# Optimization experiments

Measured on AMD Instinct MI355X. Metric: run time of the kernel, lower is better.

Reference implementation:

```python
import jax, jax.numpy as jnp
import numpy as np

EMB = 64
NEG = 0.2  # DGL GATConv default negative_slope

def seg_sum(x, ids, n):
    return jax.ops.segment_sum(x, ids, num_segments=n)

def seg_max(x, ids, n):
    return jax.ops.segment_max(x, ids, num_segments=n)

def gat(x, src, dst, W, al, ar):
    # DGL GATConv: fc (no bias), per-head additive attention, edge softmax over in-edges of dst
    N = x.shape[0]
    H, D = al.shape
    h = (x @ W).reshape(N, H, D)                 # (N,H,D)
    el = jnp.sum(h * al, -1)                     # (N,H)
    er = jnp.sum(h * ar, -1)                     # (N,H)
    e = jax.nn.leaky_relu(el[src] + er[dst], negative_slope=NEG)  # (E,H)
    m = seg_max(e, dst, N)
    ex = jnp.exp(e - m[dst])
    den = seg_sum(ex, dst, N)
    alpha = ex / den[dst]                        # (E,H)
    return seg_sum(alpha[..., None] * h[src], dst, N)  # (N,H,D)

def conv1d(x, w, b):
    y = jax.lax.conv_general_dilated(x, w, (1,), 'VALID', dimension_numbers=('NCH', 'OIH', 'NCH'))
    return y + b[None, :, None]

def maxpool1d(x, k, s):
    return jax.lax.reduce_window(x, -jnp.inf, jax.lax.max, (1, 1, k), (1, 1, s), 'VALID')

def textcnn(pad_dmap, c1w, c1b, c2w, c2b, c3w, c3b):
    x = jnp.squeeze(pad_dmap, 1).transpose(0, 2, 1)   # (B, emb, L)
    x = maxpool1d(conv1d(x, c1w, c1b), 3, 3)
    x = maxpool1d(conv1d(x, c2w, c2b), 3, 3)
    x = maxpool1d(conv1d(x, c3w, c3b), 130, 1)        # (B,128,1)
    return jnp.squeeze(x, 2)

def branch(feat, src, dst, nid, pad_dmap, ng, p):
    g = jax.nn.relu(gat(feat, src, dst, p['Wg1'], p['al1'], p['ar1'])).reshape(-1, EMB * 3)
    g = jax.nn.relu(gat(g, src, dst, p['Wg2'], p['al2'], p['ar2'])).reshape(-1, EMB * 9)
    g = jax.nn.relu(gat(g, src, dst, p['Wg3'], p['al3'], p['ar3'])).reshape(-1, EMB * 9)
    gmax = seg_max(g, nid, ng)                        # graph-level MaxPooling readout
    g = jax.nn.relu(gmax @ p['fcg_w'] + p['fcg_b'])
    s = textcnn(pad_dmap, p['c1w'], p['c1b'], p['c2w'], p['c2b'], p['c3w'], p['c3b'])
    s = jax.nn.relu(s @ p['tf_w'] + p['tf_b'])
    w = jax.nn.sigmoid(p['w1'])
    return (1.0 - w) * g + w * s

PKEYS = ['Wg1', 'al1', 'ar1', 'Wg2', 'al2', 'ar2', 'Wg3', 'al3', 'ar3', 'fcg_w', 'fcg_b',
         'c1w', 'c1b', 'c2w', 'c2b', 'c3w', 'c3b', 'tf_w', 'tf_b', 'w1',
         'fc1_w', 'fc1_b', 'fc2_w', 'fc2_b', 'out_w', 'out_b']

def forward(feat1, feat2, pad_dmap1, pad_dmap2, params, src1, dst1, src2, dst2, nid1, nid2, num_graphs):
    p = dict(zip(PKEYS, params))
    gc1 = branch(feat1, src1, dst1, nid1, pad_dmap1, num_graphs, p)
    gc2 = branch(feat2, src2, dst2, nid2, pad_dmap2, num_graphs, p)
    gc = jnp.concatenate([gc1, gc2], axis=1)
    gc = jax.nn.relu(gc @ p['fc1_w'] + p['fc1_b'])   # dropout is identity at eval
    gc = jax.nn.relu(gc @ p['fc2_w'] + p['fc2_b'])
    return jax.nn.sigmoid(gc @ p['out_w'] + p['out_b'])

def setup_inputs() -> dict:
    key = jax.random.key(0)
    ks = jax.random.split(key, 40)
    N, E, B, L = 8000, 160000, 16, 1200
    d = {}
    d['feat1'] = jax.random.normal(ks[0], (N, EMB), jnp.float32)
    d['feat2'] = jax.random.normal(ks[1], (N, EMB), jnp.float32)
    d['pad_dmap1'] = jax.random.normal(ks[2], (B, 1, L, EMB), jnp.float32)
    d['pad_dmap2'] = jax.random.normal(ks[3], (B, 1, L, EMB), jnp.float32)
    d['src1'] = jax.random.randint(ks[4], (E,), 0, N, jnp.int32)
    d['dst1'] = jax.random.randint(ks[5], (E,), 0, N, jnp.int32)
    d['src2'] = jax.random.randint(ks[6], (E,), 0, N, jnp.int32)
    d['dst2'] = jax.random.randint(ks[7], (E,), 0, N, jnp.int32)
    nid = ((jnp.arange(N) * B) // N).astype(jnp.int32)  # sorted, all graphs non-empty
    d['nid1'] = nid
    d['nid2'] = nid
    d['num_graphs'] = B
    def lin(k, i, o):
        return jax.random.normal(k, (i, o), jnp.float32) * np.float32(1.0 / np.sqrt(i))
    d['Wg1'] = lin(ks[8], EMB, EMB * 3)
    d['al1'] = jax.random.normal(ks[9], (3, EMB), jnp.float32) * 0.1
    d['ar1'] = jax.random.normal(ks[10], (3, EMB), jnp.float32) * 0.1
    d['Wg2'] = lin(ks[11], EMB * 3, EMB * 9)
    d['al2'] = jax.random.normal(ks[12], (3, EMB * 3), jnp.float32) * 0.1
    d['ar2'] = jax.random.normal(ks[13], (3, EMB * 3), jnp.float32) * 0.1
    d['Wg3'] = lin(ks[14], EMB * 9, EMB * 9)
    d['al3'] = jax.random.normal(ks[15], (1, EMB * 9), jnp.float32) * 0.1
    d['ar3'] = jax.random.normal(ks[16], (1, EMB * 9), jnp.float32) * 0.1
    d['fcg_w'] = lin(ks[17], EMB * 9, 128)
    d['fcg_b'] = jnp.zeros((128,), jnp.float32)
    d['c1w'] = jax.random.normal(ks[18], (128, EMB, 3), jnp.float32) * np.float32(1.0 / np.sqrt(EMB * 3))
    d['c1b'] = jnp.zeros((128,), jnp.float32)
    d['c2w'] = jax.random.normal(ks[19], (128, 128, 3), jnp.float32) * np.float32(1.0 / np.sqrt(128 * 3))
    d['c2b'] = jnp.zeros((128,), jnp.float32)
    d['c3w'] = jax.random.normal(ks[20], (128, 128, 3), jnp.float32) * np.float32(1.0 / np.sqrt(128 * 3))
    d['c3b'] = jnp.zeros((128,), jnp.float32)
    d['tf_w'] = lin(ks[21], 128, 128)
    d['tf_b'] = jnp.zeros((128,), jnp.float32)
    d['w1'] = jnp.full((1,), 0.5, jnp.float32)
    d['fc1_w'] = lin(ks[22], 256, 512)
    d['fc1_b'] = jnp.zeros((512,), jnp.float32)
    d['fc2_w'] = lin(ks[23], 512, 256)
    d['fc2_b'] = jnp.zeros((256,), jnp.float32)
    d['out_w'] = lin(ks[24], 256, 1)
    d['out_b'] = jnp.zeros((1,), jnp.float32)
    return d

def reference(feat1, src1, dst1, nid1, pad_dmap1, feat2, src2, dst2, nid2, pad_dmap2, num_graphs,
              Wg1, al1, ar1, Wg2, al2, ar2, Wg3, al3, ar3, fcg_w, fcg_b,
              c1w, c1b, c2w, c2b, c3w, c3b, tf_w, tf_b, w1,
              fc1_w, fc1_b, fc2_w, fc2_b, out_w, out_b):
    params = (Wg1, al1, ar1, Wg2, al2, ar2, Wg3, al3, ar3, fcg_w, fcg_b,
              c1w, c1b, c2w, c2b, c3w, c3b, tf_w, tf_b, w1,
              fc1_w, fc1_b, fc2_w, fc2_b, out_w, out_b)
    return forward(feat1, feat2, pad_dmap1, pad_dmap2, params, src1, dst1, src2, dst2, nid1, nid2, num_graphs)
```

## Files before the change

### kernel.cpp

```cpp
#include <hip/hip_runtime.h>
#include <hip/hip_bf16.h>
#include <math.h>

#define NEG_SLOPE 0.2f

__global__ void zero_i32(int* __restrict__ p, int n) {
    int i = blockIdx.x * blockDim.x + threadIdx.x;
    if (i < n) p[i] = 0;
}

__global__ void count_edges2(const int* __restrict__ dst0, const int* __restrict__ dst1,
                             int* __restrict__ cnt, int N, int E) {
    int i = blockIdx.x * blockDim.x + threadIdx.x;
    if (i >= 2 * E) return;
    int br = i >= E;
    int j = i - br * E;
    const int* d = br ? dst1 : dst0;
    atomicAdd(&cnt[br * N + d[j]], 1);
}

__global__ void scan_block(const int* __restrict__ cnt_all, int* __restrict__ rs_all, int N) {
    __shared__ int s[1024];
    int br = blockIdx.x;
    const int* cnt = cnt_all + br * N;
    int* rs = rs_all + br * (N + 1);
    int tid = threadIdx.x;
    int running = 0;
    for (int base = 0; base < N; base += 1024) {
        int v = (base + tid < N) ? cnt[base + tid] : 0;
        __syncthreads();
        s[tid] = v;
        __syncthreads();
        for (int off = 1; off < 1024; off <<= 1) {
            int t = (tid >= off) ? s[tid - off] : 0;
            __syncthreads();
            if (tid >= off) s[tid] += t;
            __syncthreads();
        }
        if (base + tid < N) rs[base + tid] = running + s[tid] - v;
        running += s[1023];
    }
    if (tid == 0) rs[N] = running;
}

__global__ void scatter_edges2(const int* __restrict__ dst0, const int* __restrict__ dst1,
                               const int* __restrict__ rs_all, int* __restrict__ fill_all,
                               int* __restrict__ eidx_all, int N, int E) {
    int i = blockIdx.x * blockDim.x + threadIdx.x;
    if (i >= 2 * E) return;
    int br = i >= E;
    int j = i - br * E;
    const int* d = br ? dst1 : dst0;
    int dd = d[j];
    int pos = atomicAdd(&fill_all[br * N + dd], 1);
    eidx_all[br * E + rs_all[br * (N + 1) + dd] + pos] = j;
}

__device__ __forceinline__ short f2bf(float x) {
    __hip_bfloat16 h = __float2bfloat16(x);
    return *reinterpret_cast<short*>(&h);
}
__device__ __forceinline__ float bf2f(short s) {
    unsigned int u = ((unsigned int)(unsigned short)s) << 16;
    return __uint_as_float(u);
}
__device__ __forceinline__ float us2f(unsigned short s) {
    return __uint_as_float((unsigned int)s << 16);
}

__global__ void split_bf2_w(const float* __restrict__ W, short* __restrict__ W2t, int K, int N) {
    int idx = blockIdx.x * blockDim.x + threadIdx.x;
    if (idx >= K * N) return;
    int k = idx / N, n = idx - k * N;
    float x = W[idx];
    short hs = f2bf(x);
    short ls = f2bf(x - bf2f(hs));
    size_t base = (size_t)n * 2 * K;
    W2t[base + k] = hs;
    W2t[base + K + k] = ls;
}

__global__ void split_bf2_cw(const float* __restrict__ w, short* __restrict__ w2, int Kp) {
    int idx = blockIdx.x * blockDim.x + threadIdx.x;
    if (idx >= 128 * Kp) return;
    int o = idx / Kp, k = idx - o * Kp;
    float x = w[idx];
    short hs = f2bf(x);
    short ls = f2bf(x - bf2f(hs));
    size_t base = (size_t)o * 2 * Kp;
    w2[base + k] = hs;
    w2[base + Kp + k] = ls;
}

typedef __attribute__((ext_vector_type(8))) short short8;
typedef __attribute__((ext_vector_type(4))) short short4v;
typedef __attribute__((ext_vector_type(4))) float floatx4;

__global__ __launch_bounds__(256) void gemm_bf3_v4(const float* __restrict__ A0,
                                                   const float* __restrict__ A1,
                                                   const short* __restrict__ Bt,
                                                   unsigned short* __restrict__ Cbf,
                                                   int M, int K, int N, size_t cBrStride) {
    __shared__ __align__(16) short sA[64 * 72];
    __shared__ __align__(16) short sB[192 * 72];
    int tid = threadIdx.x;
    int wave = tid >> 6, lane = tid & 63;
    int m = lane & 15, q = lane >> 4;
    int row0 = blockIdx.y << 6;
    int col0 = blockIdx.x * 192;
    const float* A = blockIdx.z ? A1 : A0;
    unsigned short* Cbfb = Cbf + blockIdx.z * cBrStride;
    int K2 = K * 2;
    floatx4 acc[4][3];
#pragma unroll
    for (int rt = 0; rt < 4; ++rt)
#pragma unroll
        for (int ct = 0; ct < 3; ++ct) acc[rt][ct] = (floatx4){0.f, 0.f, 0.f, 0.f};

    for (int k0 = 0; k0 < K; k0 += 32) {
#pragma unroll
        for (int p = 0; p < 2; ++p) {
            int t = tid + (p << 8);
            int r = t >> 3, c = (t & 7) << 2;
            float4 av = *(const float4*)&A[(size_t)(row0 + r) * K + k0 + c];
            short4v hs, ls;
            hs[0] = f2bf(av.x); ls[0] = f2bf(av.x - bf2f(hs[0]));
            hs[1] = f2bf(av.y); ls[1] = f2bf(av.y - bf2f(hs[1]));
            hs[2] = f2bf(av.z); ls[2] = f2bf(av.z - bf2f(hs[2]));
            hs[3] = f2bf(av.w); ls[3] = f2bf(av.w - bf2f(hs[3]));
            *(short4v*)&sA[r * 72 + c] = hs;
            *(short4v*)&sA[r * 72 + 32 + c] = ls;
        }
#pragma unroll
        for (int p = 0; p < 6; ++p) {
            int t = tid + (p << 8);
            int n = t >> 3, sub = t & 7;
            int srcoff = k0 + (sub << 3) + ((sub >= 4) ? (K - 32) : 0);
            *(float4*)&sB[n * 72 + (sub << 3)] =
                *(const float4*)&Bt[(size_t)(col0 + n) * K2 + srcoff];
        }
        __syncthreads();
        short8 a_hi[4], a_lo[4];
#pragma unroll
        for (int rt = 0; rt < 4; ++rt) {
            a_hi[rt] = *(const short8*)&sA[(rt * 16 + m) * 72 + q * 8];
            a_lo[rt] = *(const short8*)&sA[(rt * 16 + m) * 72 + 32 + q * 8];
        }
#pragma unroll
        for (int ct = 0; ct < 3; ++ct) {
            short8 b_hi = *(const short8*)&sB[(wave * 48 + ct * 16 + m) * 72 + q * 8];
            short8 b_lo = *(const short8*)&sB[(wave * 48 + ct * 16 + m) * 72 + 32 + q * 8];
#pragma unroll
            for (int rt = 0; rt < 4; ++rt) {
                acc[rt][ct] = __builtin_amdgcn_mfma_f32_16x16x32_bf16(a_hi[rt], b_hi, acc[rt][ct], 0, 0, 0);
                acc[rt][ct] = __builtin_amdgcn_mfma_f32_16x16x32_bf16(a_lo[rt], b_hi, acc[rt][ct], 0, 0, 0);
                acc[rt][ct] = __builtin_amdgcn_mfma_f32_16x16x32_bf16(a_hi[rt], b_lo, acc[rt][ct], 0, 0, 0);
            }
        }
        __syncthreads();
    }
#pragma unroll
    for (int rt = 0; rt < 4; ++rt)
#pragma unroll
        for (int ct = 0; ct < 3; ++ct)
#pragma unroll
            for (int r = 0; r < 4; ++r) {
                size_t idx = (size_t)(row0 + rt * 16 + q * 4 + r) * N + col0 + wave * 48 + ct * 16 + m;
                Cbfb[idx] = (unsigned short)f2bf(acc[rt][ct][r]);
            }
}

__global__ void gat_elr(const unsigned short* __restrict__ h, const float* __restrict__ al,
                        const float* __restrict__ ar, float* __restrict__ el,
                        float* __restrict__ er, int N, int H, int D,
                        size_t hBr, size_t eBr) {
    int wid = (blockIdx.x * blockDim.x + threadIdx.x) >> 6;
    int lane = threadIdx.x & 63;
    if (wid >= 2 * N * H) return;
    int br = wid / (N * H);
    int loc = wid - br * N * H;
    int n = loc / H, hh = loc - n * H;
    const unsigned short* hp = h + br * hBr + ((size_t)n * H + hh) * D;
    const float* alp = al + (size_t)hh * D;
    const float* arp = ar + (size_t)hh * D;
    float sl = 0.f, sr = 0.f;
    for (int d = lane; d < D; d += 64) {
        float v = us2f(hp[d]);
        sl += v * alp[d];
        sr += v * arp[d];
    }
    for (int off = 32; off > 0; off >>= 1) {
        sl += __shfl_down(sl, off, 64);
        sr += __shfl_down(sr, off, 64);
    }
    if (lane == 0) { el[br * eBr + loc] = sl; er[br * eBr + loc] = sr; }
}

__device__ __forceinline__ float lrelu(float v) {
    return (v > 0.f) ? v : NEG_SLOPE * v;
}

__global__ void gat_softmax_wave(const float* __restrict__ el_all, const float* __restrict__ er_all,
                                 const int* __restrict__ src0, const int* __restrict__ src1,
                                 const int* __restrict__ rs_all, const int* __restrict__ eidx_all,
                                 float* __restrict__ alpha_all, int N, int H, int E,
                                 size_t eBr, size_t aBr) {
    int g = (blockIdx.x * blockDim.x + threadIdx.x) >> 6;
    int lane = threadIdx.x & 63;
    if (g >= 2 * N) return;
    int br = g / N;
    int n = g - br * N;
    const int* src = br ? src1 : src0;
    const int* rs = rs_all + br * (N + 1);
    const int* eidx = eidx_all + br * E;
    const float* el = el_all + br * eBr;
    const float* er = er_all + br * eBr;
    float* alpha = alpha_all + br * aBr;
    int s0 = rs[n], s1 = rs[n + 1];
    int deg = s1 - s0;
    if (deg == 0) return;
    float ern0 = er[n * H + 0];
    float ern1 = (H > 1) ? er[n * H + 1] : 0.f;
    float ern2 = (H > 2) ? er[n * H + 2] : 0.f;
    if (deg <= 64) {
        int e = 0, s = 0;
        float v0 = -INFINITY, v1 = -INFINITY, v2 = -INFINITY;
        if (lane < deg) {
            e = eidx[s0 + lane];
            s = src[e];
            v0 = lrelu(el[s * H + 0] + ern0);
            if (H > 1) {
                v1 = lrelu(el[s * H + 1] + ern1);
                v2 = lrelu(el[s * H + 2] + ern2);
            }
        }
        float m0 = v0, m1 = v1, m2 = v2;
#pragma unroll
        for (int off = 32; off > 0; off >>= 1) {
            m0 = fmaxf(m0, __shfl_xor(m0, off, 64));
            m1 = fmaxf(m1, __shfl_xor(m1, off, 64));
            m2 = fmaxf(m2, __shfl_xor(m2, off, 64));
        }
        float ex0 = (lane < deg) ? expf(v0 - m0) : 0.f;
        float ex1 = (lane < deg && H > 1) ? expf(v1 - m1) : 0.f;
        float ex2 = (lane < deg && H > 2) ? expf(v2 - m2) : 0.f;
        float d0 = ex0, d1 = ex1, d2 = ex2;
#pragma unroll
        for (int off = 32; off > 0; off >>= 1) {
            d0 += __shfl_xor(d0, off, 64);
            d1 += __shfl_xor(d1, off, 64);
            d2 += __shfl_xor(d2, off, 64);
        }
        if (lane < deg) {
            alpha[(size_t)e * H + 0] = ex0 / d0;
            if (H > 1) {
                alpha[(size_t)e * H + 1] = ex1 / d1;
                alpha[(size_t)e * H + 2] = ex2 / d2;
            }
        }
    } else {
        float m0 = -INFINITY, m1 = -INFINITY, m2 = -INFINITY;
        for (int j = s0 + lane; j < s1; j += 64) {
            int e = eidx[j], s = src[e];
            float v0 = lrelu(el[s * H + 0] + ern0);
            alpha[(size_t)e * H + 0] = v0; m0 = fmaxf(m0, v0);
            if (H > 1) {
                float v1 = lrelu(el[s * H + 1] + ern1);
                float v2 = lrelu(el[s * H + 2] + ern2);
                alpha[(size_t)e * H + 1] = v1; m1 = fmaxf(m1, v1);
                alpha[(size_t)e * H + 2] = v2; m2 = fmaxf(m2, v2);
            }
        }
#pragma unroll
        for (int off = 32; off > 0; off >>= 1) {
            m0 = fmaxf(m0, __shfl_xor(m0, off, 64));
            m1 = fmaxf(m1, __shfl_xor(m1, off, 64));
            m2 = fmaxf(m2, __shfl_xor(m2, off, 64));
        }
        float d0 = 0.f, d1 = 0.f, d2 = 0.f;
        for (int j = s0 + lane; j < s1; j += 64) {
            int e = eidx[j];
            float ex0 = expf(alpha[(size_t)e * H + 0] - m0);
            alpha[(size_t)e * H + 0] = ex0; d0 += ex0;
            if (H > 1) {
                float ex1 = expf(alpha[(size_t)e * H + 1] - m1);
                float ex2 = expf(alpha[(size_t)e * H + 2] - m2);
                alpha[(size_t)e * H + 1] = ex1; d1 += ex1;
                alpha[(size_t)e * H + 2] = ex2; d2 += ex2;
            }
        }
#pragma unroll
        for (int off = 32; off > 0; off >>= 1) {
            d0 += __shfl_xor(d0, off, 64);
            d1 += __shfl_xor(d1, off, 64);
            d2 += __shfl_xor(d2, off, 64);
        }
        float i0 = 1.f / d0;
        float i1 = (H > 1) ? 1.f / d1 : 0.f;
        float i2 = (H > 2) ? 1.f / d2 : 0.f;
        for (int j = s0 + lane; j < s1; j += 64) {
            int e = eidx[j];
            alpha[(size_t)e * H + 0] *= i0;
            if (H > 1) {
                alpha[(size_t)e * H + 1] *= i1;
                alpha[(size_t)e * H + 2] *= i2;
            }
        }
    }
}

#define TILE_E 64
__global__ void gat_aggregate(const unsigned short* __restrict__ hb_all,
                              const float* __restrict__ alpha_all,
                              const int* __restrict__ src0, const int* __restrict__ src1,
                              const int* __restrict__ rs_all, const int* __restrict__ eidx_all,
                              float4* __restrict__ out4_all, int N, int H, int D, int E,
                              size_t hBr, size_t aBr, size_t o4Br) {
    __shared__ int s_src[TILE_E];
    __shared__ float s_alpha[TILE_E * 3];
    int n = blockIdx.x;
    int br = blockIdx.y;
    const int* src = br ? src1 : src0;
    const int* rs = rs_all + br * (N + 1);
    const int* eidx = eidx_all + br * E;
    const unsigned short* hb = hb_all + br * hBr;
    const float* alpha = alpha_all + br * aBr;
    float4* out4 = out4_all + br * o4Br;
    int HD = H * D;
    int HD4 = HD >> 2;
    int tid = threadIdx.x;
    int s0 = rs[n], s1 = rs[n + 1];
    bool active = tid < HD4;
    int hh = active ? (tid << 2) / D : 0;
    float4 acc = {0.f, 0.f, 0.f, 0.f};
    for (int base = s0; base < s1; base += TILE_E) {
        int cntE = s1 - base; if (cntE > TILE_E) cntE = TILE_E;
        if (tid < cntE) {
            int e = eidx[base + tid];
            s_src[tid] = src[e];
#pragma unroll
            for (int h = 0; h < 3; ++h)
                if (h < H) s_alpha[tid * 3 + h] = alpha[(size_t)e * H + h];
        }
        __syncthreads();
        if (active) {
#pragma unroll 4
            for (int i = 0; i < cntE; ++i) {
                float a = s_alpha[i * 3 + hh];
                ushort4 hv = *(const ushort4*)&hb[(size_t)s_src[i] * HD + (tid << 2)];
                acc.x += a * us2f(hv.x);
                acc.y += a * us2f(hv.y);
                acc.z += a * us2f(hv.z);
                acc.w += a * us2f(hv.w);
            }
        }
        __syncthreads();
    }
    if (active) {
        acc.x = fmaxf(acc.x, 0.f); acc.y = fmaxf(acc.y, 0.f);
        acc.z = fmaxf(acc.z, 0.f); acc.w = fmaxf(acc.w, 0.f);
        out4[(size_t)n * HD4 + tid] = acc;
    }
}

__global__ void seg_max_atomic(const float* __restrict__ g_all, const int* __restrict__ nid,
                               int* __restrict__ out_all, int N, int C,
                               size_t gBr, size_t oBr) {
    int br = blockIdx.y;
    const float* g = g_all + br * gBr;
    int* out = out_all + br * oBr;
    int n0 = blockIdx.x << 5;
    int n1 = n0 + 32; if (n1 > N) n1 = N;
    if (n0 >= N) return;
    for (int c = threadIdx.x; c < C; c += blockDim.x) {
        int cur = nid[n0];
        float m = 0.f;
        for (int n = n0; n < n1; ++n) {
            int gid = nid[n];
            if (gid != cur) {
                atomicMax(&out[cur * C + c], __float_as_int(m));
                cur = gid; m = 0.f;
            }
            m = fmaxf(m, g[(size_t)n * C + c]);
        }
        atomicMax(&out[cur * C + c], __float_as_int(m));
    }
}

__global__ void linear_wave(const float* __restrict__ in, const float* __restrict__ W,
                            const float* __restrict__ bias, float* __restrict__ out,
                            int K, int O, int act, size_t inBr, size_t outBr) {
    int o = blockIdx.x * 4 + (threadIdx.x >> 6);
    int b = blockIdx.y;
    int lane = threadIdx.x & 63;
    if (o >= O) return;
    const float* ip = in + blockIdx.z * inBr + (size_t)b * K;
    float acc = 0.f;
    for (int k = lane; k < K; k += 64)
        acc += ip[k] * W[(size_t)k * O + o];
    for (int off = 32; off > 0; off >>= 1)
        acc += __shfl_down(acc, off, 64);
    if (lane == 0) {
        acc += bias[o];
        if (act == 1) acc = fmaxf(acc, 0.f);
        else if (act == 2) acc = 1.f / (1.f + expf(-acc));
        out[blockIdx.z * outBr + (size_t)b * O + o] = acc;
    }
}

__global__ void transpose_pad2(const float* __restrict__ pad0, const float* __restrict__ pad1,
                               float* __restrict__ xT, int B, int L, int C) {
    int idx = blockIdx.x * blockDim.x + threadIdx.x;
    int per = B * L * C;
    if (idx >= 2 * per) return;
    int br = idx >= per;
    int loc = idx - br * per;
    const float* pad = br ? pad1 : pad0;
    int l = loc % L;
    int c = (loc / L) % C;
    int b = loc / (L * C);
    xT[idx] = pad[((size_t)b * L + l) * C + c];
}

__global__ __launch_bounds__(256) void conv_mfma(const float* __restrict__ x,
                                                 const short* __restrict__ w2,
                                                 const float* __restrict__ bias,
                                                 float* __restrict__ y,
                                                 int Cin, int Lin, int Lout,
                                                 size_t xBr, size_t yBr) {
    extern __shared__ __align__(16) char smem[];
    float* sx = (float*)smem;
    short* sB = (short*)(smem + (size_t)Cin * 68 * 4);
    int Kp = Cin * 3;
    int K2 = Kp * 2;
    int b = blockIdx.y;
    const float* xb = x + blockIdx.z * xBr + (size_t)b * Cin * Lin;
    float* yb = y + blockIdx.z * yBr + (size_t)b * 128 * Lout;
    int l0 = blockIdx.x << 6;
    int tid = threadIdx.x;
    int wave = tid >> 6, lane = tid & 63;
    int m = lane & 15, q = lane >> 4;
    int wrow = (wave & 1) << 5;
    int wcol = (wave >> 1) << 6;
    int loadL = Lin - l0; if (loadL > 66) loadL = 66;
    for (int idx = tid; idx < Cin * loadL; idx += 256) {
        int c = idx / loadL, i = idx - c * loadL;
        sx[c * 68 + i] = xb[(size_t)c * Lin + l0 + i];
    }
    floatx4 acc[2][4];
#pragma unroll
    for (int rt = 0; rt < 2; ++rt)
#pragma unroll
        for (int ct = 0; ct < 4; ++ct) acc[rt][ct] = (floatx4){0.f, 0.f, 0.f, 0.f};

    for (int k0 = 0; k0 < Kp; k0 += 32) {
#pragma unroll
        for (int p = 0; p < 4; ++p) {
            int t = tid + (p << 8);
            int o = t >> 3, slot = t & 7;
            int srcoff = k0 + ((slot & 3) << 3) + ((slot >= 4) ? Kp : 0);
            *(float4*)&sB[o * 72 + (slot << 3)] = *(const float4*)&w2[(size_t)o * K2 + srcoff];
        }
        __syncthreads();
        short8 a_hi[2], a_lo[2];
#pragma unroll
        for (int rt = 0; rt < 2; ++rt) {
            int pos = wrow + rt * 16 + m;
#pragma unroll
            for (int kk = 0; kk < 8; ++kk) {
                int k = k0 + q * 8 + kk;
                int c = k / 3, j = k - c * 3;
                float v = sx[c * 68 + pos + j];
                short hv = f2bf(v);
                a_hi[rt][kk] = hv;
                a_lo[rt][kk] = f2bf(v - bf2f(hv));
            }
        }
#pragma unroll
        for (int ct = 0; ct < 4; ++ct) {
            short8 b_hi = *(const short8*)&sB[(wcol + ct * 16 + m) * 72 + q * 8];
            short8 b_lo = *(const short8*)&sB[(wcol + ct * 16 + m) * 72 + 32 + q * 8];
#pragma unroll
            for (int rt = 0; rt < 2; ++rt) {
                acc[rt][ct] = __builtin_amdgcn_mfma_f32_16x16x32_bf16(a_hi[rt], b_hi, acc[rt][ct], 0, 0, 0);
                acc[rt][ct] = __builtin_amdgcn_mfma_f32_16x16x32_bf16(a_lo[rt], b_hi, acc[rt][ct], 0, 0, 0);
                acc[rt][ct] = __builtin_amdgcn_mfma_f32_16x16x32_bf16(a_hi[rt], b_lo, acc[rt][ct], 0, 0, 0);
            }
        }
        __syncthreads();
    }
#pragma unroll
    for (int ct = 0; ct < 4; ++ct) {
        int o = wcol + ct * 16 + m;
        float bv = bias[o];
#pragma unroll
        for (int rt = 0; rt < 2; ++rt)
#pragma unroll
            for (int r = 0; r < 4; ++r) {
                int pos = wrow + rt * 16 + q * 4 + r;
                if (l0 + pos < Lout)
                    yb[(size_t)o * Lout + l0 + pos] = acc[rt][ct][r] + bv;
            }
    }
}

__global__ void maxpool(const float* __restrict__ y, float* __restrict__ p,
                        int BC, int Lin, int k, int s, int Lout) {
    int idx = blockIdx.x * blockDim.x + threadIdx.x;
    if (idx >= BC * Lout) return;
    int lo = idx % Lout, bc = idx / Lout;
    const float* yp = y + (size_t)bc * Lin + lo * s;
    float m = -INFINITY;
    for (int i = 0; i < k; ++i) m = fmaxf(m, yp[i]);
    p[idx] = m;
}

__global__ void combine_branch2(const float* __restrict__ g, const float* __restrict__ s,
                                const float* __restrict__ w1, float* __restrict__ cat, int B) {
    int idx = blockIdx.x * blockDim.x + threadIdx.x;
    int per = B * 128;
    if (idx >= 2 * per) return;
    int br = idx >= per;
    int loc = idx - br * per;
    int b = loc >> 7, c = loc & 127;
    float w = 1.f / (1.f + expf(-w1[0]));
    cat[b * 256 + br * 128 + c] = (1.f - w) * g[idx] + w * s[idx];
}

extern "C" void kernel_launch(void* const* d_in, const int* in_sizes, int n_in,
                              void* d_out, int out_size, void* d_ws, size_t ws_size,
                              hipStream_t stream) {
    const float* feat[2] = {(const float*)d_in[0], (const float*)d_in[1]};
    const float* pad[2]  = {(const float*)d_in[2], (const float*)d_in[3]};
    const int* src[2]    = {(const int*)d_in[4], (const int*)d_in[6]};
    const int* dst[2]    = {(const int*)d_in[5], (const int*)d_in[7]};
    const int* nid[2]    = {(const int*)d_in[8], (const int*)d_in[9]};
    const float* Wg[3]   = {(const float*)d_in[11], (const float*)d_in[14], (const float*)d_in[17]};
    const float* al[3]   = {(const float*)d_in[12], (const float*)d_in[15], (const float*)d_in[18]};
    const float* ar[3]   = {(const float*)d_in[13], (const float*)d_in[16], (const float*)d_in[19]};
    const float* fcg_w = (const float*)d_in[20]; const float* fcg_b = (const float*)d_in[21];
    const float* c1w = (const float*)d_in[22];   const float* c1b = (const float*)d_in[23];
    const float* c2w = (const float*)d_in[24];   const float* c2b = (const float*)d_in[25];
    const float* c3w = (const float*)d_in[26];   const float* c3b = (const float*)d_in[27];
    const float* tf_w = (const float*)d_in[28];  const float* tf_b = (const float*)d_in[29];
    const float* w1 = (const float*)d_in[30];
    const float* fc1_w = (const float*)d_in[31]; const float* fc1_b = (const float*)d_in[32];
    const float* fc2_w = (const float*)d_in[33]; const float* fc2_b = (const float*)d_in[34];
    const float* outw = (const float*)d_in[35];  const float* outb = (const float*)d_in[36];
    float* out = (float*)d_out;

    const int N = in_sizes[0] / 64;
    const int E = in_sizes[4];
    const int B = 16, L = 1200;
    const size_t NS = (size_t)N * 576;

    char* wsb = (char*)d_ws;
    size_t off = 0;
    auto allocB = [&](size_t bytes) -> void* {
        void* p = wsb + off;
        off += (bytes + 255) & ~(size_t)255;
        return p;
    };
    auto alloc = [&](size_t elems) -> void* { return allocB(elems * 4); };

    unsigned short* h_bf = (unsigned short*)allocB(2 * NS * 2);
    float* gA    = (float*)alloc(2 * NS);
    float* el    = (float*)alloc(2 * (size_t)N * 3);
    float* er    = (float*)alloc(2 * (size_t)N * 3);
    float* alpha = (float*)alloc(2 * (size_t)E * 3);
    int* rs      = (int*)alloc(2 * (N + 1));
    int* cnt     = (int*)alloc(2 * N);
    int* eidx    = (int*)alloc(2 * E);
    int* gmax    = (int*)alloc(2 * (size_t)B * 576);
    float* gvec  = (float*)alloc(2 * (size_t)B * 128);
    float* sp    = (float*)alloc(2 * (size_t)B * 128);
    float* sf    = (float*)alloc(2 * (size_t)B * 128);
    float* cat   = (float*)alloc((size_t)B * 256);
    float* f1    = (float*)alloc((size_t)B * 512);
    float* f2    = (float*)alloc((size_t)B * 256);
    short* w2t1  = (short*)allocB((size_t)192 * 2 * 64 * 2);
    short* w2t2  = (short*)allocB((size_t)576 * 2 * 192 * 2);
    short* w2t3  = (short*)allocB((size_t)576 * 2 * 576 * 2);
    short* cw1   = (short*)allocB((size_t)128 * 2 * 192 * 2);
    short* cw2   = (short*)allocB((size_t)128 * 2 * 384 * 2);
    short* cw3   = (short*)allocB((size_t)128 * 2 * 384 * 2);
    size_t tcnn_elems = 2 * ((size_t)B * 64 * L + (size_t)B * 128 * (1198 + 399 + 397 + 132 + 130));
    size_t uni_elems = 2 * NS > tcnn_elems ? 2 * NS : tcnn_elems;
    float* uni = (float*)alloc(uni_elems);
    float* gB = uni;
    float* xT = uni;
    float* y1 = xT + 2 * (size_t)B * 64 * L;
    float* p1 = y1 + 2 * (size_t)B * 128 * 1198;
    float* y2 = p1 + 2 * (size_t)B * 128 * 399;
    float* p2 = y2 + 2 * (size_t)B * 128 * 397;
    float* y3 = p2 + 2 * (size_t)B * 128 * 132;
    (void)ws_size; (void)n_in; (void)out_size;

    split_bf2_w<<<(64 * 192 + 255) / 256, 256, 0, stream>>>(Wg[0], w2t1, 64, 192);
    split_bf2_w<<<(192 * 576 + 255) / 256, 256, 0, stream>>>(Wg[1], w2t2, 192, 576);
    split_bf2_w<<<(576 * 576 + 255) / 256, 256, 0, stream>>>(Wg[2], w2t3, 576, 576);
    split_bf2_cw<<<(128 * 192 + 255) / 256, 256, 0, stream>>>(c1w, cw1, 192);
    split_bf2_cw<<<(128 * 384 + 255) / 256, 256, 0, stream>>>(c2w, cw2, 384);
    split_bf2_cw<<<(128 * 384 + 255) / 256, 256, 0, stream>>>(c3w, cw3, 384);
    short* w2t[3] = {w2t1, w2t2, w2t3};

    zero_i32<<<(2 * N + 255) / 256, 256, 0, stream>>>(cnt, 2 * N);
    count_edges2<<<(2 * E + 255) / 256, 256, 0, stream>>>(dst[0], dst[1], cnt, N, E);
    scan_block<<<2, 1024, 0, stream>>>(cnt, rs, N);
    zero_i32<<<(2 * N + 255) / 256, 256, 0, stream>>>(cnt, 2 * N);
    scatter_edges2<<<(2 * E + 255) / 256, 256, 0, stream>>>(dst[0], dst[1], rs, cnt, eidx, N, E);

    const int dims[3][3] = {{64, 3, 64}, {192, 3, 192}, {576, 1, 576}};
    float* outs[3] = {gA, gB, gA};
    const float* inp0 = feat[0];
    const float* inp1 = feat[1];
    for (int ly = 0; ly < 3; ++ly) {
        int K = dims[ly][0], H = dims[ly][1], D = dims[ly][2];
        int HD = H * D;
        gemm_bf3_v4<<<dim3(HD / 192, N / 64, 2), 256, 0, stream>>>(inp0, inp1, w2t[ly], h_bf,
                                                                   N, K, HD, NS);
        int waves2 = 2 * N * H;
        gat_elr<<<((size_t)waves2 * 64 + 255) / 256, 256, 0, stream>>>(h_bf, al[ly], ar[ly], el, er,
                                                                       N, H, D, NS, (size_t)N * 3);
        gat_softmax_wave<<<((size_t)2 * N * 64 + 255) / 256, 256, 0, stream>>>(
            el, er, src[0], src[1], rs, eidx, alpha, N, H, E, (size_t)N * 3, (size_t)E * 3);
        int aggThreads = (((HD >> 2) + 63) / 64) * 64;
        gat_aggregate<<<dim3(N, 2), aggThreads, 0, stream>>>(
            h_bf, alpha, src[0], src[1], rs, eidx, (float4*)outs[ly],
            N, H, D, E, NS, (size_t)E * 3, NS / 4);
        inp0 = outs[ly];
        inp1 = outs[ly] + NS;
    }
    zero_i32<<<(2 * B * 576 + 255) / 256, 256, 0, stream>>>(gmax, 2 * B * 576);
    seg_max_atomic<<<dim3((N + 31) / 32, 2), 256, 0, stream>>>(gA, nid[0], gmax, N, 576,
                                                               NS, (size_t)B * 576);
    linear_wave<<<dim3(32, B, 2), 256, 0, stream>>>((const float*)gmax, fcg_w, fcg_b, gvec,
                                                    576, 128, 1, (size_t)B * 576, (size_t)B * 128);

    transpose_pad2<<<((2 * B * 64 * L) + 255) / 256, 256, 0, stream>>>(pad[0], pad[1], xT, B, L, 64);
    conv_mfma<<<dim3(19, B, 2), 256, 64 * 68 * 4 + 128 * 72 * 2, stream>>>(
        xT, cw1, c1b, y1, 64, 1200, 1198, (size_t)B * 64 * L, (size_t)B * 128 * 1198);
    maxpool<<<(2 * B * 128 * 399 + 255) / 256, 256, 0, stream>>>(y1, p1, 2 * B * 128, 1198, 3, 3, 399);
    conv_mfma<<<dim3(7, B, 2), 256, 128 * 68 * 4 + 128 * 72 * 2, stream>>>(
        p1, cw2, c2b, y2, 128, 399, 397, (size_t)B * 128 * 399, (size_t)B * 128 * 397);
    maxpool<<<(2 * B * 128 * 132 + 255) / 256, 256, 0, stream>>>(y2, p2, 2 * B * 128, 397, 3, 3, 132);
    conv_mfma<<<dim3(3, B, 2), 256, 128 * 68 * 4 + 128 * 72 * 2, stream>>>(
        p2, cw3, c3b, y3, 128, 132, 130, (size_t)B * 128 * 132, (size_t)B * 128 * 130);
    maxpool<<<(2 * B * 128 + 255) / 256, 256, 0, stream>>>(y3, sp, 2 * B * 128, 130, 130, 1, 1);
    linear_wave<<<dim3(32, B, 2), 256, 0, stream>>>(sp, tf_w, tf_b, sf, 128, 128, 1,
                                                    (size_t)B * 128, (size_t)B * 128);
    combine_branch2<<<(2 * B * 128 + 255) / 256, 256, 0, stream>>>(gvec, sf, w1, cat, B);

    linear_wave<<<dim3(128, B, 1), 256, 0, stream>>>(cat, fc1_w, fc1_b, f1, 256, 512, 1, 0, 0);
    linear_wave<<<dim3(64, B, 1), 256, 0, stream>>>(f1, fc2_w, fc2_b, f2, 512, 256, 1, 0, 0);
    linear_wave<<<dim3(1, B, 1), 256, 0, stream>>>(f2, outw, outb, out, 256, 1, 2, 0, 0);
}
```

Before: 639.2 us.

## Fuse GAT edge softmax into aggregation kernel and merge weight-split launches

Computes the per-destination edge softmax inside the aggregation block, with the first wave producing alpha values in shared memory. This removes the separate softmax kernel and the global alpha buffer round trip for each of the three layers. The six weight split kernels are also merged into one launch with hardcoded index ranges. The cost is that high-degree nodes recompute exponentials in three passes, and the other waves of each block sit idle while the softmax runs.

Measured after the change: 592.1 us. 1.08x faster.

```diff
diff --git a/kernel.cpp b/kernel.cpp
--- a/kernel.cpp
+++ b/kernel.cpp
@@ -68,9 +68,7 @@
     return __uint_as_float((unsigned int)s << 16);
 }
 
-__global__ void split_bf2_w(const float* __restrict__ W, short* __restrict__ W2t, int K, int N) {
-    int idx = blockIdx.x * blockDim.x + threadIdx.x;
-    if (idx >= K * N) return;
+__device__ __forceinline__ void split_w_elem(const float* W, short* W2t, int K, int N, int idx) {
     int k = idx / N, n = idx - k * N;
     float x = W[idx];
     short hs = f2bf(x);
@@ -79,10 +77,7 @@
     W2t[base + k] = hs;
     W2t[base + K + k] = ls;
 }
-
-__global__ void split_bf2_cw(const float* __restrict__ w, short* __restrict__ w2, int Kp) {
-    int idx = blockIdx.x * blockDim.x + threadIdx.x;
-    if (idx >= 128 * Kp) return;
+__device__ __forceinline__ void split_cw_elem(const float* w, short* w2, int Kp, int idx) {
     int o = idx / Kp, k = idx - o * Kp;
     float x = w[idx];
     short hs = f2bf(x);
@@ -90,6 +85,20 @@
     size_t base = (size_t)o * 2 * Kp;
     w2[base + k] = hs;
     w2[base + Kp + k] = ls;
+}
+__global__ void prep_weights(const float* __restrict__ Wg1, const float* __restrict__ Wg2,
+                             const float* __restrict__ Wg3, const float* __restrict__ c1w,
+                             const float* __restrict__ c2w, const float* __restrict__ c3w,
+                             short* __restrict__ w2t1, short* __restrict__ w2t2,
+                             short* __restrict__ w2t3, short* __restrict__ cw1,
+                             short* __restrict__ cw2, short* __restrict__ cw3) {
+    int idx = blockIdx.x * blockDim.x + threadIdx.x;
+    if (idx < 12288)       split_w_elem(Wg1, w2t1, 64, 192, idx);
+    else if (idx < 122880) split_w_elem(Wg2, w2t2, 192, 576, idx - 12288);
+    else if (idx < 454656) split_w_elem(Wg3, w2t3, 576, 576, idx - 122880);
+    else if (idx < 479232) split_cw_elem(c1w, cw1, 192, idx - 454656);
+    else if (idx < 528384) split_cw_elem(c2w, cw2, 384, idx - 479232);
+    else if (idx < 577536) split_cw_elem(c3w, cw3, 384, idx - 528384);
 }
 
 typedef __attribute__((ext_vector_type(8))) short short8;
@@ -200,152 +209,81 @@
     return (v > 0.f) ? v : NEG_SLOPE * v;
 }
 
-__global__ void gat_softmax_wave(const float* __restrict__ el_all, const float* __restrict__ er_all,
-                                 const int* __restrict__ src0, const int* __restrict__ src1,
-                                 const int* __restrict__ rs_all, const int* __restrict__ eidx_all,
-                                 float* __restrict__ alpha_all, int N, int H, int E,
-                                 size_t eBr, size_t aBr) {
-    int g = (blockIdx.x * blockDim.x + threadIdx.x) >> 6;
-    int lane = threadIdx.x & 63;
-    if (g >= 2 * N) return;
-    int br = g / N;
-    int n = g - br * N;
-    const int* src = br ? src1 : src0;
-    const int* rs = rs_all + br * (N + 1);
-    const int* eidx = eidx_all + br * E;
-    const float* el = el_all + br * eBr;
-    const float* er = er_all + br * eBr;
-    float* alpha = alpha_all + br * aBr;
-    int s0 = rs[n], s1 = rs[n + 1];
-    int deg = s1 - s0;
-    if (deg == 0) return;
-    float ern0 = er[n * H + 0];
-    float ern1 = (H > 1) ? er[n * H + 1] : 0.f;
-    float ern2 = (H > 2) ? er[n * H + 2] : 0.f;
-    if (deg <= 64) {
-        int e = 0, s = 0;
-        float v0 = -INFINITY, v1 = -INFINITY, v2 = -INFINITY;
-        if (lane < deg) {
-            e = eidx[s0 + lane];
-            s = src[e];
-            v0 = lrelu(el[s * H + 0] + ern0);
-            if (H > 1) {
-                v1 = lrelu(el[s * H + 1] + ern1);
-                v2 = lrelu(el[s * H + 2] + ern2);
-            }
-        }
-        float m0 = v0, m1 = v1, m2 = v2;
-#pragma unroll
-        for (int off = 32; off > 0; off >>= 1) {
-            m0 = fmaxf(m0, __shfl_xor(m0, off, 64));
-            m1 = fmaxf(m1, __shfl_xor(m1, off, 64));
-            m2 = fmaxf(m2, __shfl_xor(m2, off, 64));
-        }
-        float ex0 = (lane < deg) ? expf(v0 - m0) : 0.f;
-        float ex1 = (lane < deg && H > 1) ? expf(v1 - m1) : 0.f;
-        float ex2 = (lane < deg && H > 2) ? expf(v2 - m2) : 0.f;
-        float d0 = ex0, d1 = ex1, d2 = ex2;
-#pragma unroll
-        for (int off = 32; off > 0; off >>= 1) {
-            d0 += __shfl_xor(d0, off, 64);
-            d1 += __shfl_xor(d1, off, 64);
-            d2 += __shfl_xor(d2, off, 64);
-        }
-        if (lane < deg) {
-            alpha[(size_t)e * H + 0] = ex0 / d0;
-            if (H > 1) {
-                alpha[(size_t)e * H + 1] = ex1 / d1;
-                alpha[(size_t)e * H + 2] = ex2 / d2;
-            }
-        }
-    } else {
-        float m0 = -INFINITY, m1 = -INFINITY, m2 = -INFINITY;
-        for (int j = s0 + lane; j < s1; j += 64) {
-            int e = eidx[j], s = src[e];
-            float v0 = lrelu(el[s * H + 0] + ern0);
-            alpha[(size_t)e * H + 0] = v0; m0 = fmaxf(m0, v0);
-            if (H > 1) {
-                float v1 = lrelu(el[s * H + 1] + ern1);
-                float v2 = lrelu(el[s * H + 2] + ern2);
-                alpha[(size_t)e * H + 1] = v1; m1 = fmaxf(m1, v1);
-                alpha[(size_t)e * H + 2] = v2; m2 = fmaxf(m2, v2);
-            }
-        }
-#pragma unroll
-        for (int off = 32; off > 0; off >>= 1) {
-            m0 = fmaxf(m0, __shfl_xor(m0, off, 64));
-            m1 = fmaxf(m1, __shfl_xor(m1, off, 64));
-            m2 = fmaxf(m2, __shfl_xor(m2, off, 64));
-        }
-        float d0 = 0.f, d1 = 0.f, d2 = 0.f;
-        for (int j = s0 + lane; j < s1; j += 64) {
-            int e = eidx[j];
-            float ex0 = expf(alpha[(size_t)e * H + 0] - m0);
-            alpha[(size_t)e * H + 0] = ex0; d0 += ex0;
-            if (H > 1) {
-                float ex1 = expf(alpha[(size_t)e * H + 1] - m1);
-                float ex2 = expf(alpha[(size_t)e * H + 2] - m2);
-                alpha[(size_t)e * H + 1] = ex1; d1 += ex1;
-                alpha[(size_t)e * H + 2] = ex2; d2 += ex2;
-            }
-        }
-#pragma unroll
-        for (int off = 32; off > 0; off >>= 1) {
-            d0 += __shfl_xor(d0, off, 64);
-            d1 += __shfl_xor(d1, off, 64);
-            d2 += __shfl_xor(d2, off, 64);
-        }
-        float i0 = 1.f / d0;
-        float i1 = (H > 1) ? 1.f / d1 : 0.f;
-        float i2 = (H > 2) ? 1.f / d2 : 0.f;
-        for (int j = s0 + lane; j < s1; j += 64) {
-            int e = eidx[j];
-            alpha[(size_t)e * H + 0] *= i0;
-            if (H > 1) {
-                alpha[(size_t)e * H + 1] *= i1;
-                alpha[(size_t)e * H + 2] *= i2;
-            }
-        }
-    }
-}
-
 #define TILE_E 64
-__global__ void gat_aggregate(const unsigned short* __restrict__ hb_all,
-                              const float* __restrict__ alpha_all,
-                              const int* __restrict__ src0, const int* __restrict__ src1,
-                              const int* __restrict__ rs_all, const int* __restrict__ eidx_all,
-                              float4* __restrict__ out4_all, int N, int H, int D, int E,
-                              size_t hBr, size_t aBr, size_t o4Br) {
+__global__ void gat_softagg(const unsigned short* __restrict__ hb_all,
+                            const float* __restrict__ el_all, const float* __restrict__ er_all,
+                            const int* __restrict__ src0, const int* __restrict__ src1,
+                            const int* __restrict__ rs_all, const int* __restrict__ eidx_all,
+                            float4* __restrict__ out4_all, int N, int H, int D, int E,
+                            size_t hBr, size_t eBr, size_t o4Br) {
     __shared__ int s_src[TILE_E];
     __shared__ float s_alpha[TILE_E * 3];
+    __shared__ float s_stat[6];
     int n = blockIdx.x;
     int br = blockIdx.y;
     const int* src = br ? src1 : src0;
     const int* rs = rs_all + br * (N + 1);
     const int* eidx = eidx_all + br * E;
     const unsigned short* hb = hb_all + br * hBr;
-    const float* alpha = alpha_all + br * aBr;
+    const float* el = el_all + br * eBr;
+    const float* er = er_all + br * eBr;
     float4* out4 = out4_all + br * o4Br;
     int HD = H * D;
     int HD4 = HD >> 2;
     int tid = threadIdx.x;
     int s0 = rs[n], s1 = rs[n + 1];
-    bool active = tid < HD4;
-    int hh = active ? (tid << 2) / D : 0;
+    int deg = s1 - s0;
+    bool activeC = tid < HD4;
+    int hh = activeC ? (tid << 2) / D : 0;
     float4 acc = {0.f, 0.f, 0.f, 0.f};
-    for (int base = s0; base < s1; base += TILE_E) {
-        int cntE = s1 - base; if (cntE > TILE_E) cntE = TILE_E;
-        if (tid < cntE) {
-            int e = eidx[base + tid];
-            s_src[tid] = src[e];
-#pragma unroll
-            for (int h = 0; h < 3; ++h)
-                if (h < H) s_alpha[tid * 3 + h] = alpha[(size_t)e * H + h];
-        }
-        __syncthreads();
-        if (active) {
-#pragma unroll 4
-            for (int i = 0; i < cntE; ++i) {
+
+    if (deg > 0 && deg <= 64) {
+        if (tid < 64) {
+            int lane = tid;
+            float ern0 = er[n * H + 0];
+            float ern1 = (H > 1) ? er[n * H + 1] : 0.f;
+            float ern2 = (H > 2) ? er[n * H + 2] : 0.f;
+            int s = 0;
+            float v0 = -INFINITY, v1 = -INFINITY, v2 = -INFINITY;
+            if (lane < deg) {
+                int e = eidx[s0 + lane];
+                s = src[e];
+                v0 = lrelu(el[s * H + 0] + ern0);
+                if (H > 1) {
+                    v1 = lrelu(el[s * H + 1] + ern1);
+                    v2 = lrelu(el[s * H + 2] + ern2);
+                }
+            }
+            float m0 = v0, m1 = v1, m2 = v2;
+#pragma unroll
+            for (int off = 32; off > 0; off >>= 1) {
+                m0 = fmaxf(m0, __shfl_xor(m0, off, 64));
+                m1 = fmaxf(m1, __shfl_xor(m1, off, 64));
+                m2 = fmaxf(m2, __shfl_xor(m2, off, 64));
+            }
+            float ex0 = (lane < deg) ? expf(v0 - m0) : 0.f;
+            float ex1 = (lane < deg && H > 1) ? expf(v1 - m1) : 0.f;
+            float ex2 = (lane < deg && H > 2) ? expf(v2 - m2) : 0.f;
+            float d0 = ex0, d1 = ex1, d2 = ex2;
+#pragma unroll
+            for (int off = 32; off > 0; off >>= 1) {
+                d0 += __shfl_xor(d0, off, 64);
+                d1 += __shfl_xor(d1, off, 64);
+                d2 += __shfl_xor(d2, off, 64);
+            }
+            if (lane < deg) {
+                s_src[lane] = s;
+                s_alpha[lane * 3 + 0] = ex0 / d0;
+                if (H > 1) {
+                    s_alpha[lane * 3 + 1] = ex1 / d1;
+                    s_alpha[lane * 3 + 2] = ex2 / d2;
+                }
+            }
+        }
+        __syncthreads();
+        if (activeC) {
+#pragma unroll 8
+            for (int i = 0; i < deg; ++i) {
                 float a = s_alpha[i * 3 + hh];
                 ushort4 hv = *(const ushort4*)&hb[(size_t)s_src[i] * HD + (tid << 2)];
                 acc.x += a * us2f(hv.x);
@@ -354,9 +292,79 @@
                 acc.w += a * us2f(hv.w);
             }
         }
-        __syncthreads();
-    }
-    if (active) {
+    } else if (deg > 64) {
+        if (tid < 64) {
+            int lane = tid;
+            float ern0 = er[n * H + 0];
+            float ern1 = (H > 1) ? er[n * H + 1] : 0.f;
+            float ern2 = (H > 2) ? er[n * H + 2] : 0.f;
+            float m0 = -INFINITY, m1 = -INFINITY, m2 = -INFINITY;
+            for (int j = s0 + lane; j < s1; j += 64) {
+                int e = eidx[j], s = src[e];
+                m0 = fmaxf(m0, lrelu(el[s * H + 0] + ern0));
+                if (H > 1) {
+                    m1 = fmaxf(m1, lrelu(el[s * H + 1] + ern1));
+                    m2 = fmaxf(m2, lrelu(el[s * H + 2] + ern2));
+                }
+            }
+#pragma unroll
+            for (int off = 32; off > 0; off >>= 1) {
+                m0 = fmaxf(m0, __shfl_xor(m0, off, 64));
+                m1 = fmaxf(m1, __shfl_xor(m1, off, 64));
+                m2 = fmaxf(m2, __shfl_xor(m2, off, 64));
+            }
+            float d0 = 0.f, d1 = 0.f, d2 = 0.f;
+            for (int j = s0 + lane; j < s1; j += 64) {
+                int e = eidx[j], s = src[e];
+                d0 += expf(lrelu(el[s * H + 0] + ern0) - m0);
+                if (H > 1) {
+                    d1 += expf(lrelu(el[s * H + 1] + ern1) - m1);
+                    d2 += expf(lrelu(el[s * H + 2] + ern2) - m2);
+                }
+            }
+#pragma unroll
+            for (int off = 32; off > 0; off >>= 1) {
+                d0 += __shfl_xor(d0, off, 64);
+                d1 += __shfl_xor(d1, off, 64);
+                d2 += __shfl_xor(d2, off, 64);
+            }
+            if (lane == 0) {
+                s_stat[0] = m0; s_stat[1] = m1; s_stat[2] = m2;
+                s_stat[3] = 1.f / d0;
+                s_stat[4] = (H > 1) ? 1.f / d1 : 0.f;
+                s_stat[5] = (H > 2) ? 1.f / d2 : 0.f;
+            }
+        }
+        __syncthreads();
+        float m0 = s_stat[0], m1 = s_stat[1], m2 = s_stat[2];
+        float i0 = s_stat[3], i1 = s_stat[4], i2 = s_stat[5];
+        for (int base = s0; base < s1; base += TILE_E) {
+            int cnt = s1 - base; if (cnt > TILE_E) cnt = TILE_E;
+            __syncthreads();
+            if (tid < cnt) {
+                int e = eidx[base + tid], s = src[e];
+                s_src[tid] = s;
+                s_alpha[tid * 3 + 0] = expf(lrelu(el[s * H + 0] + er[n * H + 0]) - m0) * i0;
+                if (H > 1) {
+                    s_alpha[tid * 3 + 1] = expf(lrelu(el[s * H + 1] + er[n * H + 1]) - m1) * i1;
+                    s_alpha[tid * 3 + 2] = expf(lrelu(el[s * H + 2] + er[n * H + 2]) - m2) * i2;
+                }
+            }
+            __syncthreads();
+            if (activeC) {
+#pragma unroll 4
+                for (int i = 0; i < cnt; ++i) {
+                    float a = s_alpha[i * 3 + hh];
+                    ushort4 hv = *(const ushort4*)&hb[(size_t)s_src[i] * HD + (tid << 2)];
+                    acc.x += a * us2f(hv.x);
+                    acc.y += a * us2f(hv.y);
+                    acc.z += a * us2f(hv.z);
+                    acc.w += a * us2f(hv.w);
+                }
+            }
+        }
+    }
+    if (activeC) {
         acc.x = fmaxf(acc.x, 0.f); acc.y = fmaxf(acc.y, 0.f);
         acc.z = fmaxf(acc.z, 0.f); acc.w = fmaxf(acc.w, 0.f);
         out4[(size_t)n * HD4 + tid] = acc;
@@ -567,7 +575,6 @@
     float* gA    = (float*)alloc(2 * NS);
     float* el    = (float*)alloc(2 * (size_t)N * 3);
     float* er    = (float*)alloc(2 * (size_t)N * 3);
-    float* alpha = (float*)alloc(2 * (size_t)E * 3);
     int* rs      = (int*)alloc(2 * (N + 1));
     int* cnt     = (int*)alloc(2 * N);
     int* eidx    = (int*)alloc(2 * E);
@@ -596,12 +603,8 @@
     float* y3 = p2 + 2 * (size_t)B * 128 * 132;
     (void)ws_size; (void)n_in; (void)out_size;
 
-    split_bf2_w<<<(64 * 192 + 255) / 256, 256, 0, stream>>>(Wg[0], w2t1, 64, 192);
-    split_bf2_w<<<(192 * 576 + 255) / 256, 256, 0, stream>>>(Wg[1], w2t2, 192, 576);
-    split_bf2_w<<<(576 * 576 + 255) / 256, 256, 0, stream>>>(Wg[2], w2t3, 576, 576);
-    split_bf2_cw<<<(128 * 192 + 255) / 256, 256, 0, stream>>>(c1w, cw1, 192);
-    split_bf2_cw<<<(128 * 384 + 255) / 256, 256, 0, stream>>>(c2w, cw2, 384);
-    split_bf2_cw<<<(128 * 384 + 255) / 256, 256, 0, stream>>>(c3w, cw3, 384);
+    prep_weights<<<2256, 256, 0, stream>>>(Wg[0], Wg[1], Wg[2], c1w, c2w, c3w,
+                                           w2t1, w2t2, w2t3, cw1, cw2, cw3);
     short* w2t[3] = {w2t1, w2t2, w2t3};
 
     zero_i32<<<(2 * N + 255) / 256, 256, 0, stream>>>(cnt, 2 * N);
@@ -622,12 +625,10 @@
         int waves2 = 2 * N * H;
         gat_elr<<<((size_t)waves2 * 64 + 255) / 256, 256, 0, stream>>>(h_bf, al[ly], ar[ly], el, er,
                                                                        N, H, D, NS, (size_t)N * 3);
-        gat_softmax_wave<<<((size_t)2 * N * 64 + 255) / 256, 256, 0, stream>>>(
-            el, er, src[0], src[1], rs, eidx, alpha, N, H, E, (size_t)N * 3, (size_t)E * 3);
         int aggThreads = (((HD >> 2) + 63) / 64) * 64;
-        gat_aggregate<<<dim3(N, 2), aggThreads, 0, stream>>>(
-            h_bf, alpha, src[0], src[1], rs, eidx, (float4*)outs[ly],
-            N, H, D, E, NS, (size_t)E * 3, NS / 4);
+        gat_softagg<<<dim3(N, 2), aggThreads, 0, stream>>>(
+            h_bf, el, er, src[0], src[1], rs, eidx, (float4*)outs[ly],
+            N, H, D, E, NS, (size_t)N * 3, NS / 4);
         inp0 = outs[ly];
         inp1 = outs[ly] + NS;
     }
```
